# Optimization experiments

Measured on AMD Instinct MI355X. Metric: run time of the kernel, lower is better.

Reference implementation:

```python
import jax, jax.numpy as jnp
import numpy as np

NUM_HEADS = 16
SLICE_SIZE = 1024
SCALING = SLICE_SIZE ** 0.5  # module divides by sqrt(slice_size), as written


def setup_inputs() -> dict:
    key = jax.random.key(0)
    ks = jax.random.split(key, 9)
    B, S, D = 4, 2048, SLICE_SIZE
    sc = 0.02
    return {
        "x": jax.random.normal(ks[0], (B, S, D), dtype=jnp.float32),
        "Wq": jax.random.normal(ks[1], (D, D), dtype=jnp.float32) * sc,
        "bq": jax.random.normal(ks[2], (D,), dtype=jnp.float32) * sc,
        "Wk": jax.random.normal(ks[3], (D, D), dtype=jnp.float32) * sc,
        "bk": jax.random.normal(ks[4], (D,), dtype=jnp.float32) * sc,
        "Wv": jax.random.normal(ks[5], (D, D), dtype=jnp.float32) * sc,
        "bv": jax.random.normal(ks[6], (D,), dtype=jnp.float32) * sc,
        "Wp": jax.random.normal(ks[7], (D, D), dtype=jnp.float32) * sc,
        "bp": jax.random.normal(ks[8], (D,), dtype=jnp.float32) * sc,
    }


def _split_heads(t):
    # 'b s (h o) -> b h s o'
    b, s, d = t.shape
    return t.reshape(b, s, NUM_HEADS, d // NUM_HEADS).transpose(0, 2, 1, 3)


def reference(x, Wq, bq, Wk, bk, Wv, bv, Wp, bp):
    q = _split_heads(x @ Wq.T + bq)  # [B,H,S,O]
    k = _split_heads(x @ Wk.T + bk)
    v = _split_heads(x @ Wv.T + bv)
    energy = jnp.einsum('bhqo,bhko->bhqk', q, k)  # full score matrix
    attn = jax.nn.softmax(energy / SCALING, axis=-1)
    # Faithful to source: 'b h q k, b h v o -> b h v o' sums attn over (q,k)
    out = jnp.einsum('bhqk,bhvo->bhvo', attn, v)
    b, h, s, o = out.shape
    out = out.transpose(0, 2, 1, 3).reshape(b, s, h * o)  # 'b h v o -> b v (h o)'
    return out @ Wp.T + bp
```

## Files before the change

### kernel.cpp

```cpp
#include <hip/hip_runtime.h>
#include <cstdint>


typedef unsigned short u16;
typedef __bf16 bf16x8 __attribute__((ext_vector_type(8)));
typedef float f32x4 __attribute__((ext_vector_type(4)));

__device__ __forceinline__ u16 f2bf(float f) {
  unsigned int u = __float_as_uint(f);
  u += 0x7fffu + ((u >> 16) & 1u);
  return (u16)(u >> 16);
}

__device__ __forceinline__ void load16(const void* g, void* l) {
  auto gp = (const __attribute__((address_space(1))) unsigned int*)(uintptr_t)g;
  auto lp = (__attribute__((address_space(3))) unsigned int*)(unsigned int)(uintptr_t)l;
  __builtin_amdgcn_global_load_lds(gp, lp, 16, 0, 0);
}

__global__ void k_prep(const float* __restrict__ x, const float* __restrict__ Wv,
                       const float* __restrict__ bv, const float* __restrict__ Wp,
                       const float* __restrict__ bp, u16* __restrict__ xb,
                       u16* __restrict__ wpb, u16* __restrict__ wvtb,
                       float* __restrict__ cv) {
  __shared__ float tile[32][33];
  const int b = blockIdx.x;
  const int tid = threadIdx.x;
  if (b < 9216) {
    const float* src = (b < 8192) ? x : Wp;
    u16* dst = (b < 8192) ? xb : wpb;
    const long base = (long)((b < 8192) ? b : (b - 8192)) * 1024 + tid * 4;
    const float4 v = *(const float4*)(src + base);
    ushort4 o;
    o.x = f2bf(v.x); o.y = f2bf(v.y); o.z = f2bf(v.z); o.w = f2bf(v.w);
    *(ushort4*)(dst + base) = o;
  } else if (b < 10240) {
    const int tb = b - 9216;
    const int bi = (tb & 31) * 32;
    const int bj = (tb >> 5) * 32;
    const int tx = tid & 31;
    const int ty = tid >> 5;
    for (int r = ty; r < 32; r += 8)
      tile[r][tx] = Wv[(long)(bj + r) * 1024 + bi + tx];
    __syncthreads();
    for (int r = ty; r < 32; r += 8)
      wvtb[(long)(bi + r) * 1024 + bj + tx] = f2bf(tile[tx][r]);
  } else {
    const int row = (b - 10240) * 4 + (tid >> 6);
    const int lane = tid & 63;
    const float* w = Wp + (long)row * 1024;
    float s = 0.f;
    for (int j = lane; j < 1024; j += 64) s += w[j] * bv[j];
    for (int off = 32; off; off >>= 1) s += __shfl_down(s, off, 64);
    if (lane == 0) cv[row] = 2048.f * s + bp[row];
  }
}

__global__ void k_reduce(const float* __restrict__ p, u16* __restrict__ dst) {
  const long i = (long)(blockIdx.x * 256 + threadIdx.x) * 4;
  const float4 a = *(const float4*)(p + i);
  const float4 b = *(const float4*)(p + 1048576 + i);
  const float4 c = *(const float4*)(p + 2097152 + i);
  const float4 d = *(const float4*)(p + 3145728 + i);
  ushort4 o;
  o.x = f2bf((a.x + b.x + c.x + d.x) * 2048.f);
  o.y = f2bf((a.y + b.y + c.y + d.y) * 2048.f);
  o.z = f2bf((a.z + b.z + c.z + d.z) * 2048.f);
  o.w = f2bf((a.w + b.w + c.w + d.w) * 2048.f);
  *(ushort4*)(dst + i) = o;
}

template <int MODE>
__global__ __launch_bounds__(256, 2) void k_gemm(
    const u16* __restrict__ A, const u16* __restrict__ B, float* __restrict__ Out,
    const float* __restrict__ bias, int M, int N, int K) {
  __shared__ u16 As[128 * 128];
  __shared__ u16 Bs[128 * 128];

  const int tid = threadIdx.x;
  const int lane = tid & 63;
  const int wv = tid >> 6;
  const int waveM = (wv & 1) << 6;
  const int waveN = (wv >> 1) << 6;
  const int l15 = lane & 15;
  const int quad = lane >> 4;

  long bm, bn;
  int kBeg, kEnd;
  if constexpr (MODE == 0) {
    const int id = blockIdx.x;
    const int xcd = id & 7;
    const int j = id >> 3;
    const int nb = N >> 7;
    const int mPerXcd = M / 128 / 8;
    bm = (long)(xcd * mPerXcd + j / nb) * 128;
    bn = (long)(j % nb) * 128;
    kBeg = 0; kEnd = K;
  } else {
    bm = (long)blockIdx.x * 128;
    bn = (long)blockIdx.y * 128;
    const int kChunk = K / gridDim.z;
    kBeg = blockIdx.z * kChunk;
    kEnd = kBeg + kChunk;
  }

  const int rr = (wv << 2) + (lane >> 4);
  const int s15 = lane & 15;
  const int kc = s15 ^ (rr & 7);
  const u16* Ag = A + (bm + rr) * (long)K + kc * 8;
  const u16* Bg = B + (bn + rr) * (long)K + kc * 8;
  u16* Asw = As + (wv << 9);
  u16* Bsw = Bs + (wv << 9);

  const f32x4 zero = {0.f, 0.f, 0.f, 0.f};
  f32x4 acc[4][4];
#pragma unroll
  for (int i = 0; i < 4; ++i)
#pragma unroll
    for (int j = 0; j < 4; ++j) acc[i][j] = zero;

  for (int k0 = kBeg; k0 < kEnd; k0 += 128) {
    __syncthreads();
#pragma unroll
    for (int r = 0; r < 8; ++r)
      load16(Ag + (long)(r * 16) * K + k0, Asw + r * 2048);
#pragma unroll
    for (int r = 0; r < 8; ++r)
      load16(Bg + (long)(r * 16) * K + k0, Bsw + r * 2048);
    __syncthreads();

#pragma unroll
    for (int kk = 0; kk < 4; ++kk) {
      const int swz = ((kk << 2) + quad) ^ (l15 & 7);
      bf16x8 af[4], bg[4];
#pragma unroll
      for (int t = 0; t < 4; ++t) {
        af[t] = *(const bf16x8*)(As + (waveM + t * 16 + l15) * 128 + swz * 8);
        bg[t] = *(const bf16x8*)(Bs + (waveN + t * 16 + l15) * 128 + swz * 8);
      }
#pragma unroll
      for (int i = 0; i < 4; ++i)
#pragma unroll
        for (int j = 0; j < 4; ++j)
          acc[i][j] = __builtin_amdgcn_mfma_f32_16x16x32_bf16(af[i], bg[j], acc[i][j], 0, 0, 0);
    }
  }

  float* outp = (MODE == 1) ? Out + (long)blockIdx.z * M * N : Out;
#pragma unroll
  for (int i = 0; i < 4; ++i) {
    const long gm = bm + waveM + i * 16 + quad * 4;
#pragma unroll
    for (int j = 0; j < 4; ++j) {
      const long gn = bn + waveN + j * 16 + l15;
      const float bb = (MODE == 0) ? bias[gn] : 0.f;
#pragma unroll
      for (int r = 0; r < 4; ++r)
        outp[(gm + r) * N + gn] = acc[i][j][r] + bb;
    }
  }
}

extern "C" void kernel_launch(void* const* d_in, const int* in_sizes, int n_in,
                              void* d_out, int out_size, void* d_ws, size_t ws_size,
                              hipStream_t stream) {
  const float* x  = (const float*)d_in[0];
  const float* Wv = (const float*)d_in[5];
  const float* bv = (const float*)d_in[6];
  const float* Wp = (const float*)d_in[7];
  const float* bp = (const float*)d_in[8];

  char* ws = (char*)d_ws;
  u16* xb    = (u16*)(ws);
  u16* wpb   = (u16*)(ws + (16u << 20));
  u16* wvtb  = (u16*)(ws + (18u << 20));
  u16* m2b   = (u16*)(ws + (20u << 20));
  float* cv  = (float*)(ws + (22u << 20));
  float* m2f = (float*)(ws + (22u << 20) + 4096);

  k_prep<<<10496, 256, 0, stream>>>(x, Wv, bv, Wp, bp, xb, wpb, wvtb, cv);

  k_gemm<1><<<dim3(8, 8, 4), 256, 0, stream>>>(wpb, wvtb, m2f, nullptr,
                                               1024, 1024, 1024);
  k_reduce<<<1024, 256, 0, stream>>>(m2f, m2b);

  k_gemm<0><<<512, 256, 0, stream>>>(xb, m2b, (float*)d_out, cv,
                                     8192, 1024, 1024);
}
```

Before: 143.0 us.

## Double-buffer GEMM LDS tiles and drop split-K reduce kernel

Rewrites the GEMM main loop to use 64-wide K tiles in two LDS buffers, so the next tile's global loads are issued before the MFMAs on the current tile. The small weight-product GEMM no longer uses split-K plus a separate reduce kernel. It now runs as 64 blocks over the full K and writes scaled bf16 directly, which removes one launch and an fp32 round trip. The cost is that the small GEMM runs with far fewer blocks, and the min-occupancy launch bound is dropped.

```diff
diff --git a/kernel.cpp b/kernel.cpp
--- a/kernel.cpp
+++ b/kernel.cpp
@@ -56,26 +56,12 @@
   }
 }
 
-__global__ void k_reduce(const float* __restrict__ p, u16* __restrict__ dst) {
-  const long i = (long)(blockIdx.x * 256 + threadIdx.x) * 4;
-  const float4 a = *(const float4*)(p + i);
-  const float4 b = *(const float4*)(p + 1048576 + i);
-  const float4 c = *(const float4*)(p + 2097152 + i);
-  const float4 d = *(const float4*)(p + 3145728 + i);
-  ushort4 o;
-  o.x = f2bf((a.x + b.x + c.x + d.x) * 2048.f);
-  o.y = f2bf((a.y + b.y + c.y + d.y) * 2048.f);
-  o.z = f2bf((a.z + b.z + c.z + d.z) * 2048.f);
-  o.w = f2bf((a.w + b.w + c.w + d.w) * 2048.f);
-  *(ushort4*)(dst + i) = o;
-}
-
 template <int MODE>
-__global__ __launch_bounds__(256, 2) void k_gemm(
-    const u16* __restrict__ A, const u16* __restrict__ B, float* __restrict__ Out,
+__global__ __launch_bounds__(256) void k_gemm(
+    const u16* __restrict__ A, const u16* __restrict__ B, void* __restrict__ OutV,
     const float* __restrict__ bias, int M, int N, int K) {
-  __shared__ u16 As[128 * 128];
-  __shared__ u16 Bs[128 * 128];
+  __shared__ u16 As[2][128 * 64];
+  __shared__ u16 Bs[2][128 * 64];
 
   const int tid = threadIdx.x;
   const int lane = tid & 63;
@@ -86,7 +72,6 @@
   const int quad = lane >> 4;
 
   long bm, bn;
-  int kBeg, kEnd;
   if constexpr (MODE == 0) {
     const int id = blockIdx.x;
     const int xcd = id & 7;
@@ -95,22 +80,27 @@
     const int mPerXcd = M / 128 / 8;
     bm = (long)(xcd * mPerXcd + j / nb) * 128;
     bn = (long)(j % nb) * 128;
-    kBeg = 0; kEnd = K;
   } else {
-    bm = (long)blockIdx.x * 128;
-    bn = (long)blockIdx.y * 128;
-    const int kChunk = K / gridDim.z;
-    kBeg = blockIdx.z * kChunk;
-    kEnd = kBeg + kChunk;
+    bm = (long)(blockIdx.x >> 3) * 128;
+    bn = (long)(blockIdx.x & 7) * 128;
   }
 
-  const int rr = (wv << 2) + (lane >> 4);
-  const int s15 = lane & 15;
-  const int kc = s15 ^ (rr & 7);
-  const u16* Ag = A + (bm + rr) * (long)K + kc * 8;
-  const u16* Bg = B + (bn + rr) * (long)K + kc * 8;
-  u16* Asw = As + (wv << 9);
-  u16* Bsw = Bs + (wv << 9);
+  const int rsl = lane >> 3;
+  const int cs = (lane & 7) ^ rsl;
+  const u16* Ag0 = A + (bm + wv * 8 + rsl) * (long)K + cs * 8;
+  const u16* Bg0 = B + (bn + wv * 8 + rsl) * (long)K + cs * 8;
+
+  const int nT = K >> 6;
+
+  auto STAGE = [&](long k0, int b) {
+    u16* Ad = &As[b][0] + (wv << 9);
+    u16* Bd = &Bs[b][0] + (wv << 9);
+#pragma unroll
+    for (int r = 0; r < 4; ++r) {
+      load16(Ag0 + k0 + (long)(r * 32) * K, Ad + (r << 11));
+      load16(Bg0 + k0 + (long)(r * 32) * K, Bd + (r << 11));
+    }
+  };
 
   const f32x4 zero = {0.f, 0.f, 0.f, 0.f};
   f32x4 acc[4][4];
@@ -119,44 +109,68 @@
 #pragma unroll
     for (int j = 0; j < 4; ++j) acc[i][j] = zero;
 
-  for (int k0 = kBeg; k0 < kEnd; k0 += 128) {
-    __syncthreads();
+  const int rq0 = quad ^ (l15 & 7);
+  const int rq1 = (4 + quad) ^ (l15 & 7);
+
+  STAGE(0, 0);
+  asm volatile("s_waitcnt vmcnt(0)" ::: "memory");
+  __builtin_amdgcn_s_barrier();
+
+  int cur = 0;
+  for (int t = 0; t < nT; ++t) {
+    const bool more = (t + 1) < nT;
+    if (more) STAGE((long)(t + 1) << 6, cur ^ 1);
+    __builtin_amdgcn_sched_barrier(0);
+
+    const u16* Asb = &As[cur][0];
+    const u16* Bsb = &Bs[cur][0];
+    bf16x8 af[2][4], bg[2][4];
 #pragma unroll
-    for (int r = 0; r < 8; ++r)
-      load16(Ag + (long)(r * 16) * K + k0, Asw + r * 2048);
-#pragma unroll
-    for (int r = 0; r < 8; ++r)
-      load16(Bg + (long)(r * 16) * K + k0, Bsw + r * 2048);
-    __syncthreads();
+    for (int tt = 0; tt < 4; ++tt) {
+      const int ra = (waveM + tt * 16 + l15) * 64;
+      const int rb = (waveN + tt * 16 + l15) * 64;
+      af[0][tt] = *(const bf16x8*)(Asb + ra + rq0 * 8);
+      af[1][tt] = *(const bf16x8*)(Asb + ra + rq1 * 8);
+      bg[0][tt] = *(const bf16x8*)(Bsb + rb + rq0 * 8);
+      bg[1][tt] = *(const bf16x8*)(Bsb + rb + rq1 * 8);
+    }
+    asm volatile("s_waitcnt lgkmcnt(0)" ::: "memory");
+    __builtin_amdgcn_sched_barrier(0);
 
 #pragma unroll
-    for (int kk = 0; kk < 4; ++kk) {
-      const int swz = ((kk << 2) + quad) ^ (l15 & 7);
-      bf16x8 af[4], bg[4];
-#pragma unroll
-      for (int t = 0; t < 4; ++t) {
-        af[t] = *(const bf16x8*)(As + (waveM + t * 16 + l15) * 128 + swz * 8);
-        bg[t] = *(const bf16x8*)(Bs + (waveN + t * 16 + l15) * 128 + swz * 8);
-      }
+    for (int kk = 0; kk < 2; ++kk)
 #pragma unroll
       for (int i = 0; i < 4; ++i)
 #pragma unroll
         for (int j = 0; j < 4; ++j)
-          acc[i][j] = __builtin_amdgcn_mfma_f32_16x16x32_bf16(af[i], bg[j], acc[i][j], 0, 0, 0);
+          acc[i][j] = __builtin_amdgcn_mfma_f32_16x16x32_bf16(af[kk][i], bg[kk][j],
+                                                              acc[i][j], 0, 0, 0);
+
+    if (more) {
+      asm volatile("s_waitcnt vmcnt(0)" ::: "memory");
+      __builtin_amdgcn_s_barrier();
+      cur ^= 1;
     }
   }
 
-  float* outp = (MODE == 1) ? Out + (long)blockIdx.z * M * N : Out;
 #pragma unroll
   for (int i = 0; i < 4; ++i) {
     const long gm = bm + waveM + i * 16 + quad * 4;
 #pragma unroll
     for (int j = 0; j < 4; ++j) {
       const long gn = bn + waveN + j * 16 + l15;
-      const float bb = (MODE == 0) ? bias[gn] : 0.f;
+      if constexpr (MODE == 0) {
+        float* outp = (float*)OutV;
+        const float bb = bias[gn];
 #pragma unroll
-      for (int r = 0; r < 4; ++r)
-        outp[(gm + r) * N + gn] = acc[i][j][r] + bb;
+        for (int r = 0; r < 4; ++r)
+          outp[(gm + r) * N + gn] = acc[i][j][r] + bb;
+      } else {
+        u16* outp = (u16*)OutV;
+#pragma unroll
+        for (int r = 0; r < 4; ++r)
+          outp[(gm + r) * N + gn] = f2bf(acc[i][j][r] * 2048.f);
+      }
     }
   }
 }
@@ -176,14 +190,10 @@
   u16* wvtb  = (u16*)(ws + (18u << 20));
   u16* m2b   = (u16*)(ws + (20u << 20));
   float* cv  = (float*)(ws + (22u << 20));
-  float* m2f = (float*)(ws + (22u << 20) + 4096);
 
   k_prep<<<10496, 256, 0, stream>>>(x, Wv, bv, Wp, bp, xb, wpb, wvtb, cv);
 
-  k_gemm<1><<<dim3(8, 8, 4), 256, 0, stream>>>(wpb, wvtb, m2f, nullptr,
-                                               1024, 1024, 1024);
-  k_reduce<<<1024, 256, 0, stream>>>(m2f, m2b);
+  k_gemm<1><<<64, 256, 0, stream>>>(wpb, wvtb, m2b, nullptr, 1024, 1024, 1024);
 
-  k_gemm<0><<<512, 256, 0, stream>>>(xb, m2b, (float*)d_out, cv,
-                                     8192, 1024, 1024);
+  k_gemm<0><<<512, 256, 0, stream>>>(xb, m2b, d_out, cv, 8192, 1024, 1024);
 }
```

New measurement: 140.5 us. About the same (-1.7%).
